# Kernel tuning notes

Measured on AMD Instinct MI355X. Metric: run time of the kernel, lower is better.

Reference implementation:

```python
import jax, jax.numpy as jnp
import numpy as np

NUM_REL = 5000
NUM_BIN = 32
NUM_EDGES = 200000
DIM = 512
NUM_HEAD = 8
DIM_HID = DIM // NUM_HEAD


def setup_inputs() -> dict:
    key = jax.random.key(0)
    ks = jax.random.split(key, 10)
    emb_rel = jax.random.normal(ks[0], (NUM_REL, DIM), dtype=jnp.float32)
    emb_bin = jax.random.normal(ks[1], (NUM_BIN, DIM), dtype=jnp.float32)
    head = jax.random.randint(ks[2], (NUM_EDGES, 1), 0, NUM_REL)
    tail = jax.random.randint(ks[3], (NUM_EDGES, 1), 0, NUM_REL)
    bins = jax.random.randint(ks[4], (NUM_EDGES, 1), 0, NUM_BIN)
    relation_triplets = jnp.concatenate([head, tail, bins], axis=1).astype(jnp.int64)
    gain = float(np.sqrt(2.0))  # calculate_gain('relu')
    # xavier normal: std = gain * sqrt(2/(fan_in+fan_out))
    std_attn = gain * np.sqrt(2.0 / (3 * DIM + DIM))
    std_aggr = gain * np.sqrt(2.0 / (DIM + DIM))
    std_vec = gain * np.sqrt(2.0 / (NUM_HEAD + DIM_HID))
    W_attn = std_attn * jax.random.normal(ks[5], (DIM, 3 * DIM), dtype=jnp.float32)
    b_attn = jnp.zeros((DIM,), dtype=jnp.float32)
    attn_vec = std_vec * jax.random.normal(ks[6], (1, NUM_HEAD, DIM_HID), dtype=jnp.float32)
    W_aggr = std_aggr * jax.random.normal(ks[7], (DIM, DIM), dtype=jnp.float32)
    b_aggr = jnp.zeros((DIM,), dtype=jnp.float32)
    return {"emb_rel": emb_rel, "emb_bin": emb_bin, "relation_triplets": relation_triplets,
            "W_attn": W_attn, "b_attn": b_attn, "attn_vec": attn_vec,
            "W_aggr": W_aggr, "b_aggr": b_aggr}


def reference(emb_rel, emb_bin, relation_triplets, W_attn, b_attn, attn_vec, W_aggr, b_aggr):
    num_rel = emb_rel.shape[0]
    head = relation_triplets[:, 0]
    tail = relation_triplets[:, 1]
    bins = relation_triplets[:, 2]
    # gather + concat -> [E, 3*D]
    concat = jnp.concatenate([emb_rel[head], emb_bin[bins], emb_rel[tail]], axis=-1)
    h = jax.nn.leaky_relu(concat @ W_attn.T + b_attn, negative_slope=0.2)
    h = h.reshape(-1, NUM_HEAD, DIM_HID)
    attn_raw = jnp.sum(h * attn_vec, axis=-1)  # [E, H]
    # segmented softmax over edges sharing the same head relation
    seg_max = jax.ops.segment_max(attn_raw, head, num_segments=num_rel)  # [R, H]
    seg_max = jnp.where(jnp.isfinite(seg_max), seg_max, 0.0)  # empty segments
    ev = jnp.exp(attn_raw - seg_max[head])  # [E, H]
    seg_sum = jax.ops.segment_sum(ev, head, num_segments=num_rel)  # [R, H]
    beta = ev / (seg_sum[head] + 1e-16)  # [E, H]
    msg = (emb_rel[tail] @ W_aggr.T + b_aggr).reshape(-1, NUM_HEAD, DIM_HID)  # [E, H, Dh]
    out = jax.ops.segment_sum(beta[..., None] * msg, head, num_segments=num_rel)  # [R, H, Dh]
    return out.reshape(num_rel, -1)
```

## Files before the change

kernel.cpp:

```cpp
#include <hip/hip_runtime.h>
#include <hip/hip_bf16.h>

#define NREL 5000
#define NBIN 32
#define NEDGE 200000
#define DIM 512
#define NHEAD 8
#define CAP 256

typedef __attribute__((ext_vector_type(8))) short short8;
typedef __attribute__((ext_vector_type(4))) short short4v;
typedef __attribute__((ext_vector_type(4))) float f32x4;
typedef unsigned short ushort_t;

#define REL_N (NREL * DIM)
#define BIN_N (NBIN * DIM)
#define WATTN_N (DIM * 3 * DIM)
#define WAGGR_N (DIM * DIM)
#define CTOT (REL_N + BIN_N + WATTN_N + WAGGR_N)
#define CONV_BLOCKS (CTOT / 4 / 256)

__device__ __forceinline__ float b2f(ushort_t u) {
  unsigned int v = ((unsigned int)u) << 16;
  union { unsigned int i; float f; } c; c.i = v; return c.f;
}
__device__ __forceinline__ ushort_t f2b_rne(float f) {
  union { float f; unsigned int u; } c; c.f = f;
  unsigned int u = c.u;
  return (ushort_t)((u + 0x7FFFu + ((u >> 16) & 1u)) >> 16);
}
__device__ __forceinline__ void gload16(const void* g, void* l) {
  __builtin_amdgcn_global_load_lds(
      (const __attribute__((address_space(1))) void*)g,
      (__attribute__((address_space(3))) void*)l, 16, 0, 0);
}
template<int CTRL>
__device__ __forceinline__ float dpp_add(float x) {
  int v = __builtin_amdgcn_update_dpp(0, __float_as_int(x), CTRL, 0xF, 0xF, true);
  return x + __int_as_float(v);
}

__global__ void conv_k(const float* __restrict__ s_rel, const float* __restrict__ s_bin,
                       const float* __restrict__ s_wattn, const float* __restrict__ s_waggr,
                       ushort_t* __restrict__ dst, int* __restrict__ cur) {
  int b = blockIdx.x;
  if (b < 20) {
    int i = b * 256 + threadIdx.x;
    if (i < NREL) cur[i] = 0;
  }
  const int O1 = REL_N, O2 = O1 + BIN_N, O3 = O2 + WATTN_N;
  int i4 = (b * 256 + threadIdx.x) * 4;
  const float* src; int j;
  if (i4 < O1)      { src = s_rel;   j = i4; }
  else if (i4 < O2) { src = s_bin;   j = i4 - O1; }
  else if (i4 < O3) { src = s_wattn; j = i4 - O2; }
  else              { src = s_waggr; j = i4 - O3; }
  float4 v = *(const float4*)(src + j);
  short4v o;
  o[0] = (short)f2b_rne(v.x); o[1] = (short)f2b_rne(v.y);
  o[2] = (short)f2b_rne(v.z); o[3] = (short)f2b_rne(v.w);
  *(short4v*)(dst + i4) = o;
}

__global__ __launch_bounds__(256) void gemm_scatter_k(
    const ushort_t* __restrict__ c_rel, const ushort_t* __restrict__ c_bin,
    const ushort_t* __restrict__ c_wattn, const float* __restrict__ b_attn,
    const ushort_t* __restrict__ c_waggr, const float* __restrict__ b_aggr,
    ushort_t* __restrict__ P1B, ushort_t* __restrict__ PM, ushort_t* __restrict__ P2,
    const int* __restrict__ trip, int* __restrict__ cur, unsigned int* __restrict__ etb)
{
  __shared__ ushort_t Alds[64 * 64];
  __shared__ ushort_t Blds[128 * 64];
  int bx = blockIdx.x, by = blockIdx.y;
  if (by >= 12) {
    int sid = (by - 12) * 80 + bx;
    for (int i = threadIdx.x; i < 625; i += 256) {
      int e = sid * 625 + i;
      int h  = trip[3 * e];
      int ta = trip[3 * e + 1];
      int bi = trip[3 * e + 2];
      h  = min(max(h, 0), NREL - 1);
      ta = min(max(ta, 0), NREL - 1);
      bi = min(max(bi, 0), NBIN - 1);
      int p = atomicAdd(&cur[h], 1);
      if (p < CAP)
        etb[(h << 8) + p] = ((unsigned int)ta << 11) | ((unsigned int)bi << 24);
    }
    return;
  }
  const ushort_t* A; int Arows;
  const ushort_t* Bbase; int Bld; int joff;
  const float* bias;
  ushort_t* OUT; int OUTld; int ocolOff;
  int rbase;
  if (bx == 79) {
    if (by >= 4) return;
    A = c_bin; Arows = NBIN; rbase = 0;
    Bbase = c_wattn + 512; Bld = 3 * DIM; joff = 0;
    bias = b_attn;
    OUT = P2; OUTld = DIM; ocolOff = 0;
  } else {
    A = c_rel; Arows = NREL; rbase = bx * 64;
    int seg = by >> 2;
    if (seg == 2)      { Bbase = c_waggr;        Bld = DIM;     bias = b_aggr; }
    else if (seg == 1) { Bbase = c_wattn + 1024; Bld = 3 * DIM; bias = nullptr; }
    else               { Bbase = c_wattn;        Bld = 3 * DIM; bias = nullptr; }
    joff = seg * 512;
    OUT = (seg == 0) ? P1B : PM;
    OUTld = (seg == 0) ? DIM : 1024;
    ocolOff = (seg == 0) ? 0 : 512;
  }
  int tid = threadIdx.x;
  int l = tid & 63, wv = tid >> 6;
  int ctb = by * 128;
  int lr = l >> 3;
  int srcslot = (l & 7) ^ lr;
  const ushort_t* aS0; const ushort_t* aS1;
  const ushort_t* bS0; const ushort_t* bS1; const ushort_t* bS2; const ushort_t* bS3;
  {
    int a0 = wv * 16 + 0 * 8 + lr, a1 = wv * 16 + 1 * 8 + lr;
    aS0 = A + (size_t)min(rbase + a0, Arows - 1) * DIM + srcslot * 8;
    aS1 = A + (size_t)min(rbase + a1, Arows - 1) * DIM + srcslot * 8;
    int c0 = wv * 32 + 0 * 8 + lr, c1 = wv * 32 + 1 * 8 + lr,
        c2 = wv * 32 + 2 * 8 + lr, c3 = wv * 32 + 3 * 8 + lr;
    bS0 = Bbase + (size_t)(ctb + c0 - joff) * Bld + srcslot * 8;
    bS1 = Bbase + (size_t)(ctb + c1 - joff) * Bld + srcslot * 8;
    bS2 = Bbase + (size_t)(ctb + c2 - joff) * Bld + srcslot * 8;
    bS3 = Bbase + (size_t)(ctb + c3 - joff) * Bld + srcslot * 8;
  }
  ushort_t* aD0 = Alds + (wv * 16 + 0) * 64;
  ushort_t* aD1 = Alds + (wv * 16 + 8) * 64;
  ushort_t* bD0 = Blds + (wv * 32 + 0) * 64;
  ushort_t* bD1 = Blds + (wv * 32 + 8) * 64;
  ushort_t* bD2 = Blds + (wv * 32 + 16) * 64;
  ushort_t* bD3 = Blds + (wv * 32 + 24) * 64;

  f32x4 acc[4][2] = {};
  for (int kk = 0; kk < DIM; kk += 64) {
    gload16(aS0 + kk, aD0); gload16(aS1 + kk, aD1);
    gload16(bS0 + kk, bD0); gload16(bS1 + kk, bD1);
    gload16(bS2 + kk, bD2); gload16(bS3 + kk, bD3);
    __syncthreads();
#pragma unroll
    for (int ks = 0; ks < 2; ++ks) {
      int sg = ks * 4 + (l >> 4);
      int sw = (sg ^ (l & 7)) * 8;
      short8 aF[4], bF[2];
#pragma unroll
      for (int m2 = 0; m2 < 4; ++m2) {
        int mrow = m2 * 16 + (l & 15);
        aF[m2] = *(const short8*)(Alds + mrow * 64 + sw);
      }
#pragma unroll
      for (int n = 0; n < 2; ++n) {
        int crow = wv * 32 + n * 16 + (l & 15);
        bF[n] = *(const short8*)(Blds + crow * 64 + sw);
      }
#pragma unroll
      for (int m2 = 0; m2 < 4; ++m2)
#pragma unroll
        for (int n = 0; n < 2; ++n)
          acc[m2][n] = __builtin_amdgcn_mfma_f32_16x16x32_bf16(aF[m2], bF[n], acc[m2][n], 0, 0, 0);
    }
    __syncthreads();
  }
  int r0 = rbase + (l >> 4) * 4;
#pragma unroll
  for (int n = 0; n < 2; ++n) {
    int col = ctb + wv * 32 + n * 16 + (l & 15);
    float bv = bias ? bias[col - joff] : 0.0f;
    int ocol = col - ocolOff;
#pragma unroll
    for (int m2 = 0; m2 < 4; ++m2) {
#pragma unroll
      for (int jj = 0; jj < 4; ++jj) {
        int row = r0 + m2 * 16 + jj;
        if (row < Arows) OUT[(size_t)row * OUTld + ocol] = f2b_rne(acc[m2][n][jj] + bv);
      }
    }
  }
}

#define EDGE_LOAD(TB, P2V, P3V, MV)                                     \
  {                                                                     \
    const char* row_ = PMc + ((TB) & 0x00FFFFFFu);                      \
    P2V = *(const short8*)(p2lds + (((TB) >> 24) << 10) + l16);         \
    P3V = *(const short8*)(row_ + l16);                                 \
    MV  = *(const short8*)(row_ + 1024 + l16);                          \
  }

#define EDGE_COMPUTE(P2V, P3V, MV)                                      \
  {                                                                     \
    float part = 0.0f;                                                  \
    _Pragma("unroll")                                                   \
    for (int j = 0; j < 8; ++j) {                                       \
      float z = p1v[j] + b2f((ushort_t)P2V[j]) + b2f((ushort_t)P3V[j]); \
      part += z * (z > 0.f ? avv[j] : avv02[j]);                        \
    }                                                                   \
    part = dpp_add<0xB1>(part);        \
    part = dpp_add<0x4E>(part);        \
    part += __shfl_xor(part, 4);                                        \
    if (part > m + 8.0f) {                                              \
      float f = __expf(m - part);                                       \
      s *= f;                                                           \
      _Pragma("unroll")                                                 \
      for (int j = 0; j < 8; ++j) acc[j] *= f;                          \
      m = part;                                                         \
    }                                                                   \
    float ev = __expf(part - m);                                        \
    s += ev;                                                            \
    _Pragma("unroll")                                                   \
    for (int j = 0; j < 8; ++j) acc[j] += ev * b2f((ushort_t)MV[j]);    \
  }

__global__ __launch_bounds__(256, 6) void aggr2_k(
    const int* __restrict__ cur, const unsigned int* __restrict__ etb,
    const ushort_t* __restrict__ P1B, const ushort_t* __restrict__ PM,
    const ushort_t* __restrict__ P2, const float* __restrict__ avec,
    float* __restrict__ outf)
{
  __shared__ __align__(16) char shmem[32 * DIM * 2];

  int t = threadIdx.x;
  int l = t & 63, wv = t >> 6;
  int p = wv >> 1, sub = wv & 1;
  int r = blockIdx.x * 2 + p;
  int nE = min(cur[r], CAP);
  int base = r << 8;
  int half = nE >> 1;
  int start = sub ? half : 0;
  int cnt = sub ? (nE - half) : half;

  int hd1 = l >> 3;
  int ob = l * 8;
  int l16 = l * 16;

  {
    ushort_t* p2dst = (ushort_t*)shmem;
#pragma unroll
    for (int i = 0; i < 8; ++i) {
      int idx = t * 8 + i * 2048;
      *(short8*)(p2dst + idx) = *(const short8*)(P2 + idx);
    }
  }

  float p1v[8], avv[8], avv02[8];
  {
    short8 p1b = *(const short8*)(P1B + (size_t)r * DIM + ob);
#pragma unroll
    for (int j = 0; j < 8; ++j) {
      p1v[j] = b2f((ushort_t)p1b[j]);
      float a = avec[ob + j];
      avv[j] = a;
      avv02[j] = 0.2f * a;
    }
  }
  float acc[8] = {};
  float m = -INFINITY, s = 0.0f;

  const char* PMc = (const char*)PM;
  const char* p2lds = (const char*)shmem;

  __syncthreads();

  for (int ck = 0; ck < cnt; ck += 64) {
    int ne = min(64, cnt - ck);
    unsigned int tbreg = 0;
    if (l < ne) tbreg = etb[base + start + ck + l];
    short8 p2A, p3A, mvA, p2B, p3B, mvB;
    unsigned int tb0 = (unsigned int)__shfl((int)tbreg, 0);
    EDGE_LOAD(tb0, p2A, p3A, mvA);
    int i = 0;
    while (i + 1 < ne) {
      unsigned int tbb = (unsigned int)__shfl((int)tbreg, i + 1);
      EDGE_LOAD(tbb, p2B, p3B, mvB);
      EDGE_COMPUTE(p2A, p3A, mvA);
      if (i + 2 < ne) {
        unsigned int tba = (unsigned int)__shfl((int)tbreg, i + 2);
        EDGE_LOAD(tba, p2A, p3A, mvA);
      }
      EDGE_COMPUTE(p2B, p3B, mvB);
      i += 2;
    }
    if (i < ne) EDGE_COMPUTE(p2A, p3A, mvA);
  }

  __syncthreads();
  float* red = (float*)shmem;
  float* ms  = (float*)(shmem + 8192);
#pragma unroll
  for (int j = 0; j < 8; ++j) red[wv * DIM + ob + j] = acc[j];
  if ((l & 7) == 0) { ms[(wv * NHEAD + hd1) * 2] = m; ms[(wv * NHEAD + hd1) * 2 + 1] = s; }
  __syncthreads();

  int pp = t >> 7;
  int d0 = (t & 127) * 4;
  int h = d0 >> 6;
  int rr = blockIdx.x * 2 + pp;
  float m1 = ms[((2 * pp) * NHEAD + h) * 2],     s1 = ms[((2 * pp) * NHEAD + h) * 2 + 1];
  float m2 = ms[((2 * pp + 1) * NHEAD + h) * 2], s2 = ms[((2 * pp + 1) * NHEAD + h) * 2 + 1];
  float M = fmaxf(m1, m2);
  float c1 = (m1 == M) ? 1.0f : __expf(m1 - M);
  float c2 = (m2 == M) ? 1.0f : __expf(m2 - M);
  float S = s1 * c1 + s2 * c2;
  float inv = 1.0f / (S + 1e-16f);
  float4 val;
  val.x = (red[(2 * pp) * DIM + d0]     * c1 + red[(2 * pp + 1) * DIM + d0]     * c2) * inv;
  val.y = (red[(2 * pp) * DIM + d0 + 1] * c1 + red[(2 * pp + 1) * DIM + d0 + 1] * c2) * inv;
  val.z = (red[(2 * pp) * DIM + d0 + 2] * c1 + red[(2 * pp + 1) * DIM + d0 + 2] * c2) * inv;
  val.w = (red[(2 * pp) * DIM + d0 + 3] * c1 + red[(2 * pp + 1) * DIM + d0 + 3] * c2) * inv;
  *(float4*)(outf + (size_t)rr * DIM + d0) = val;
}

extern "C" void kernel_launch(void* const* d_in, const int* in_sizes, int n_in,
                              void* d_out, int out_size, void* d_ws, size_t ws_size,
                              hipStream_t stream) {
  const float* s_rel   = (const float*)d_in[0];
  const float* s_bin   = (const float*)d_in[1];
  const int*   trip    = (const int*)d_in[2];
  const float* s_wattn = (const float*)d_in[3];
  const float* b_attn  = (const float*)d_in[4];
  const float* avec    = (const float*)d_in[5];
  const float* s_waggr = (const float*)d_in[6];
  const float* b_aggr  = (const float*)d_in[7];

  ushort_t* canon = (ushort_t*)d_ws;
  ushort_t* c_rel   = canon;
  ushort_t* c_bin   = c_rel + REL_N;
  ushort_t* c_wattn = c_bin + BIN_N;
  ushort_t* c_waggr = c_wattn + WATTN_N;
  int* cur = (int*)(c_waggr + WAGGR_N);
  unsigned int* etb = (unsigned int*)(cur + NREL);
  ushort_t* P1B = (ushort_t*)(((uintptr_t)(etb + NREL * CAP) + 15) & ~(uintptr_t)15);
  ushort_t* PM  = P1B + (size_t)NREL * DIM;
  ushort_t* P2  = PM + (size_t)NREL * 1024;

  conv_k<<<CONV_BLOCKS, 256, 0, stream>>>(s_rel, s_bin, s_wattn, s_waggr, canon, cur);

  dim3 gg(80, 16);
  gemm_scatter_k<<<gg, 256, 0, stream>>>(c_rel, c_bin, c_wattn, b_attn, c_waggr, b_aggr,
                                         P1B, PM, P2, trip, cur, etb);

  aggr2_k<<<NREL / 2, 256, 0, stream>>>(cur, etb, P1B, PM, P2, avec, (float*)d_out);
}
```

Measured before the change: 80.89 us.

## Split each wave into two half-waves processing separate edges with wider per-lane slices

Each wave now splits into two 32-lane halves, each handling a different edge at once. Every lane covers 16 features instead of 8, with 32-byte loads and four independent partial sums, and the head reduction no longer needs a cross-lane shuffle. The explicit two-stage software prefetch is removed, the final merge combines four online-softmax partial states per row instead of two, and launch bounds drop from 6 to 4 blocks per SM. Intent is more edges in flight and fewer reduction steps, at the cost of more registers, lower occupancy and no explicit load/compute overlap.

Result: slower. 83.42 us (+3.1%).

```diff
diff --git a/kernel.cpp b/kernel.cpp
--- a/kernel.cpp
+++ b/kernel.cpp
@@ -181,39 +181,7 @@
   }
 }
 
-#define EDGE_LOAD(TB, P2V, P3V, MV)                                     \
-  {                                                                     \
-    const char* row_ = PMc + ((TB) & 0x00FFFFFFu);                      \
-    P2V = *(const short8*)(p2lds + (((TB) >> 24) << 10) + l16);         \
-    P3V = *(const short8*)(row_ + l16);                                 \
-    MV  = *(const short8*)(row_ + 1024 + l16);                          \
-  }
-
-#define EDGE_COMPUTE(P2V, P3V, MV)                                      \
-  {                                                                     \
-    float part = 0.0f;                                                  \
-    _Pragma("unroll")                                                   \
-    for (int j = 0; j < 8; ++j) {                                       \
-      float z = p1v[j] + b2f((ushort_t)P2V[j]) + b2f((ushort_t)P3V[j]); \
-      part += z * (z > 0.f ? avv[j] : avv02[j]);                        \
-    }                                                                   \
-    part = dpp_add<0xB1>(part);        \
-    part = dpp_add<0x4E>(part);        \
-    part += __shfl_xor(part, 4);                                        \
-    if (part > m + 8.0f) {                                              \
-      float f = __expf(m - part);                                       \
-      s *= f;                                                           \
-      _Pragma("unroll")                                                 \
-      for (int j = 0; j < 8; ++j) acc[j] *= f;                          \
-      m = part;                                                         \
-    }                                                                   \
-    float ev = __expf(part - m);                                        \
-    s += ev;                                                            \
-    _Pragma("unroll")                                                   \
-    for (int j = 0; j < 8; ++j) acc[j] += ev * b2f((ushort_t)MV[j]);    \
-  }
-
-__global__ __launch_bounds__(256, 6) void aggr2_k(
+__global__ __launch_bounds__(256, 4) void aggr2_k(
     const int* __restrict__ cur, const unsigned int* __restrict__ etb,
     const ushort_t* __restrict__ P1B, const ushort_t* __restrict__ PM,
     const ushort_t* __restrict__ P2, const float* __restrict__ avec,
@@ -224,6 +192,8 @@
   int t = threadIdx.x;
   int l = t & 63, wv = t >> 6;
   int p = wv >> 1, sub = wv & 1;
+  int g = l >> 5;
+  int ll = l & 31;
   int r = blockIdx.x * 2 + p;
   int nE = min(cur[r], CAP);
   int base = r << 8;
@@ -231,9 +201,9 @@
   int start = sub ? half : 0;
   int cnt = sub ? (nE - half) : half;
 
-  int hd1 = l >> 3;
-  int ob = l * 8;
-  int l16 = l * 16;
+  int hd1 = ll >> 2;
+  int ob = ll * 16;
+  int b32 = ll * 32;
 
   {
     ushort_t* p2dst = (ushort_t*)shmem;
@@ -244,18 +214,19 @@
     }
   }
 
-  float p1v[8], avv[8], avv02[8];
+  float p1v[16], avv[16];
   {
-    short8 p1b = *(const short8*)(P1B + (size_t)r * DIM + ob);
+    short8 pa = *(const short8*)(P1B + (size_t)r * DIM + ob);
+    short8 pb = *(const short8*)(P1B + (size_t)r * DIM + ob + 8);
 #pragma unroll
     for (int j = 0; j < 8; ++j) {
-      p1v[j] = b2f((ushort_t)p1b[j]);
-      float a = avec[ob + j];
-      avv[j] = a;
-      avv02[j] = 0.2f * a;
-    }
-  }
-  float acc[8] = {};
+      p1v[j] = b2f((ushort_t)pa[j]);
+      p1v[j + 8] = b2f((ushort_t)pb[j]);
+    }
+#pragma unroll
+    for (int j = 0; j < 16; ++j) avv[j] = avec[ob + j];
+  }
+  float acc[16] = {};
   float m = -INFINITY, s = 0.0f;
 
   const char* PMc = (const char*)PM;
@@ -267,48 +238,82 @@
     int ne = min(64, cnt - ck);
     unsigned int tbreg = 0;
     if (l < ne) tbreg = etb[base + start + ck + l];
-    short8 p2A, p3A, mvA, p2B, p3B, mvB;
-    unsigned int tb0 = (unsigned int)__shfl((int)tbreg, 0);
-    EDGE_LOAD(tb0, p2A, p3A, mvA);
-    int i = 0;
-    while (i + 1 < ne) {
-      unsigned int tbb = (unsigned int)__shfl((int)tbreg, i + 1);
-      EDGE_LOAD(tbb, p2B, p3B, mvB);
-      EDGE_COMPUTE(p2A, p3A, mvA);
-      if (i + 2 < ne) {
-        unsigned int tba = (unsigned int)__shfl((int)tbreg, i + 2);
-        EDGE_LOAD(tba, p2A, p3A, mvA);
+    for (int k = 0; 2 * k < ne; ++k) {
+      int idx = 2 * k + g;
+      unsigned int tb = (unsigned int)__shfl((int)tbreg, idx);
+      if (idx < ne) {
+        const char* row_ = PMc + (tb & 0x00FFFFFFu);
+        const char* p2r = p2lds + ((tb >> 24) << 10) + b32;
+        short8 p2a = *(const short8*)(p2r);
+        short8 p2b = *(const short8*)(p2r + 16);
+        short8 p3a = *(const short8*)(row_ + b32);
+        short8 p3b = *(const short8*)(row_ + b32 + 16);
+        short8 mva = *(const short8*)(row_ + 1024 + b32);
+        short8 mvb = *(const short8*)(row_ + 1024 + b32 + 16);
+        float pt0 = 0.f, pt1 = 0.f, pt2 = 0.f, pt3 = 0.f;
+#pragma unroll
+        for (int j = 0; j < 4; ++j) {
+          float z0 = p1v[j]      + b2f((ushort_t)p2a[j])     + b2f((ushort_t)p3a[j]);
+          float z1 = p1v[j + 4]  + b2f((ushort_t)p2a[j + 4]) + b2f((ushort_t)p3a[j + 4]);
+          float z2 = p1v[j + 8]  + b2f((ushort_t)p2b[j])     + b2f((ushort_t)p3b[j]);
+          float z3 = p1v[j + 12] + b2f((ushort_t)p2b[j + 4]) + b2f((ushort_t)p3b[j + 4]);
+          pt0 += z0 * (z0 > 0.f ? avv[j]      : 0.2f * avv[j]);
+          pt1 += z1 * (z1 > 0.f ? avv[j + 4]  : 0.2f * avv[j + 4]);
+          pt2 += z2 * (z2 > 0.f ? avv[j + 8]  : 0.2f * avv[j + 8]);
+          pt3 += z3 * (z3 > 0.f ? avv[j + 12] : 0.2f * avv[j + 12]);
+        }
+        float part = (pt0 + pt1) + (pt2 + pt3);
+        part = dpp_add<0xB1>(part);
+        part = dpp_add<0x4E>(part);
+        if (part > m + 8.0f) {
+          float f = __expf(m - part);
+          s *= f;
+#pragma unroll
+          for (int j = 0; j < 16; ++j) acc[j] *= f;
+          m = part;
+        }
+        float ev = __expf(part - m);
+        s += ev;
+#pragma unroll
+        for (int j = 0; j < 8; ++j) acc[j] += ev * b2f((ushort_t)mva[j]);
+#pragma unroll
+        for (int j = 0; j < 8; ++j) acc[j + 8] += ev * b2f((ushort_t)mvb[j]);
       }
-      EDGE_COMPUTE(p2B, p3B, mvB);
-      i += 2;
-    }
-    if (i < ne) EDGE_COMPUTE(p2A, p3A, mvA);
+    }
   }
 
   __syncthreads();
   float* red = (float*)shmem;
-  float* ms  = (float*)(shmem + 8192);
-#pragma unroll
-  for (int j = 0; j < 8; ++j) red[wv * DIM + ob + j] = acc[j];
-  if ((l & 7) == 0) { ms[(wv * NHEAD + hd1) * 2] = m; ms[(wv * NHEAD + hd1) * 2 + 1] = s; }
+  float* ms  = (float*)(shmem + 16384);
+  int q = p * 4 + sub * 2 + g;
+#pragma unroll
+  for (int j = 0; j < 16; ++j) red[q * DIM + ob + j] = acc[j];
+  if ((ll & 3) == 0) { ms[(q * NHEAD + hd1) * 2] = m; ms[(q * NHEAD + hd1) * 2 + 1] = s; }
   __syncthreads();
 
   int pp = t >> 7;
   int d0 = (t & 127) * 4;
   int h = d0 >> 6;
   int rr = blockIdx.x * 2 + pp;
-  float m1 = ms[((2 * pp) * NHEAD + h) * 2],     s1 = ms[((2 * pp) * NHEAD + h) * 2 + 1];
-  float m2 = ms[((2 * pp + 1) * NHEAD + h) * 2], s2 = ms[((2 * pp + 1) * NHEAD + h) * 2 + 1];
-  float M = fmaxf(m1, m2);
+  int q0 = pp * 4;
+  float m0 = ms[((q0)     * NHEAD + h) * 2], s0 = ms[((q0)     * NHEAD + h) * 2 + 1];
+  float m1 = ms[((q0 + 1) * NHEAD + h) * 2], s1 = ms[((q0 + 1) * NHEAD + h) * 2 + 1];
+  float m2 = ms[((q0 + 2) * NHEAD + h) * 2], s2 = ms[((q0 + 2) * NHEAD + h) * 2 + 1];
+  float m3 = ms[((q0 + 3) * NHEAD + h) * 2], s3 = ms[((q0 + 3) * NHEAD + h) * 2 + 1];
+  float M = fmaxf(fmaxf(m0, m1), fmaxf(m2, m3));
+  float c0 = (m0 == M) ? 1.0f : __expf(m0 - M);
   float c1 = (m1 == M) ? 1.0f : __expf(m1 - M);
   float c2 = (m2 == M) ? 1.0f : __expf(m2 - M);
-  float S = s1 * c1 + s2 * c2;
+  float c3 = (m3 == M) ? 1.0f : __expf(m3 - M);
+  float S = s0 * c0 + s1 * c1 + s2 * c2 + s3 * c3;
   float inv = 1.0f / (S + 1e-16f);
   float4 val;
-  val.x = (red[(2 * pp) * DIM + d0]     * c1 + red[(2 * pp + 1) * DIM + d0]     * c2) * inv;
-  val.y = (red[(2 * pp) * DIM + d0 + 1] * c1 + red[(2 * pp + 1) * DIM + d0 + 1] * c2) * inv;
-  val.z = (red[(2 * pp) * DIM + d0 + 2] * c1 + red[(2 * pp + 1) * DIM + d0 + 2] * c2) * inv;
-  val.w = (red[(2 * pp) * DIM + d0 + 3] * c1 + red[(2 * pp + 1) * DIM + d0 + 3] * c2) * inv;
+#pragma unroll
+  for (int dj = 0; dj < 4; ++dj) {
+    float v = red[q0 * DIM + d0 + dj] * c0 + red[(q0 + 1) * DIM + d0 + dj] * c1 +
+              red[(q0 + 2) * DIM + d0 + dj] * c2 + red[(q0 + 3) * DIM + d0 + dj] * c3;
+    ((float*)&val)[dj] = v * inv;
+  }
   *(float4*)(outf + (size_t)rr * DIM + d0) = val;
 }
 
```
